# Kernel tuning notes

Hardware: AMD Instinct MI355X
Metric: run time of the kernel (lower is better)

## Reference

```python
import jax, jax.numpy as jnp
import numpy as np

B, S, D = 2, 2048, 1024
H = 16
DH = D // H  # 64

def setup_inputs() -> dict:
    key = jax.random.key(0)
    k1, k2, k3, k4 = jax.random.split(key, 4)
    scale = 0.02
    x = jax.random.normal(k1, (B, S, D), dtype=jnp.float32)
    W_query = jax.random.normal(k2, (D, D), dtype=jnp.float32) * scale
    W_key = jax.random.normal(k3, (D, D), dtype=jnp.float32) * scale
    W_value = jax.random.normal(k4, (D, D), dtype=jnp.float32) * scale
    return {"x": x, "W_query": W_query, "W_key": W_key, "W_value": W_value}

def reference(x, W_query, W_key, W_value):
    b, n, d_in = x.shape
    # project and split heads: [b, h, n, dh]
    q = (x @ W_query).reshape(b, n, H, DH).transpose(0, 2, 1, 3)
    k = (x @ W_key).reshape(b, n, H, DH).transpose(0, 2, 1, 3)
    v = (x @ W_value).reshape(b, n, H, DH).transpose(0, 2, 1, 3)
    # raw scores, then causal mask (strict upper triangle -> -inf)
    scores = jnp.einsum('bhqd,bhkd->bhqk', q, k)
    causal = jnp.tril(jnp.ones((n, n), dtype=bool))  # True = keep
    scores = jnp.where(causal, scores, -jnp.inf)
    weights = jax.nn.softmax(scores / jnp.sqrt(jnp.float32(DH)), axis=-1)
    ctx = jnp.einsum('bhqk,bhkd->bhqd', weights, v)
    return ctx.transpose(0, 2, 1, 3).reshape(b, n, H * DH)
```

## Files before the change

### kernel.cpp

```cpp
#include <hip/hip_runtime.h>
#include <hip/hip_bf16.h>

#define S_LEN   2048
#define D_MODEL 1024
#define N_HEADS 16
#define D_HEAD  64
#define HEAD_ELEMS (2048ull * 64ull)
#define MAT_ELEMS  (4096ull * 1024ull)
#define W_ELEMS    (1024ull * 1024ull)

typedef __attribute__((ext_vector_type(8))) short short8_t;
typedef __attribute__((ext_vector_type(4))) short short4_t;
typedef __attribute__((ext_vector_type(4))) float f32x4;

__device__ __forceinline__ short f2bf(float f) {
    __hip_bfloat16 h = __float2bfloat16(f);
    union { __hip_bfloat16 h; short s; } cv;
    cv.h = h;
    return cv.s;
}

#define GLD_LDS16(gptr, lptr) \
    __builtin_amdgcn_global_load_lds( \
        (const __attribute__((address_space(1))) unsigned int*)(gptr), \
        (__attribute__((address_space(3))) unsigned int*)(lptr), 16, 0, 0)

__global__ __launch_bounds__(256) void convert_x_kernel(
    const float* __restrict__ x, short* __restrict__ xb)
{
    const int i = (blockIdx.x * 256 + threadIdx.x) * 8;
    const float4 v0 = *(const float4*)(x + i);
    const float4 v1 = *(const float4*)(x + i + 4);
    short8_t u;
    u[0] = f2bf(v0.x); u[1] = f2bf(v0.y); u[2] = f2bf(v0.z); u[3] = f2bf(v0.w);
    u[4] = f2bf(v1.x); u[5] = f2bf(v1.y); u[6] = f2bf(v1.z); u[7] = f2bf(v1.w);
    *(short8_t*)(xb + i) = u;
}

__global__ __launch_bounds__(256) void transpose_w_kernel(
    const float* __restrict__ Wq, const float* __restrict__ Wk,
    const float* __restrict__ Wv, short* __restrict__ wt)
{
    const int k0 = blockIdx.x * 64;
    const int n0 = blockIdx.y * 64;
    const int which = blockIdx.z;
    const float* W = (which == 0) ? Wq : (which == 1) ? Wk : Wv;
    short* out = wt + (size_t)which * W_ELEMS;

    __shared__ float Ts[64][68];
    const int t = threadIdx.x;
    {
        const int c4 = (t & 15) * 4;
#pragma unroll
        for (int i = 0; i < 4; ++i) {
            const int r = (t >> 4) + i * 16;
            const float4 v = *(const float4*)(W + (size_t)(k0 + r) * D_MODEL + n0 + c4);
            Ts[c4 + 0][r] = v.x; Ts[c4 + 1][r] = v.y;
            Ts[c4 + 2][r] = v.z; Ts[c4 + 3][r] = v.w;
        }
    }
    __syncthreads();
    const int nl = t >> 2;
#pragma unroll
    for (int s = 0; s < 2; ++s) {
        const int koff = (t & 3) * 8 + s * 32;
        short8_t u;
#pragma unroll
        for (int j = 0; j < 8; ++j) u[j] = f2bf(Ts[nl][koff + j]);
        *(short8_t*)(out + (size_t)(n0 + nl) * D_MODEL + k0 + koff) = u;
    }
}

__global__ __launch_bounds__(256, 3) void qkv_mfma_gemm_kernel(
    const short* __restrict__ xb,
    const short* __restrict__ wt,
    short* __restrict__ qkv)
{
    const int mBlock = blockIdx.x * 128;
    const int nBlock = blockIdx.y * 128;
    const int which  = blockIdx.z;
    const short* Bt = wt + (size_t)which * W_ELEMS;
    short* outBase  = qkv + (size_t)which * MAT_ELEMS;

    __shared__ short As[128 * 32];
    __shared__ short Bs[128 * 32];

    const int t    = threadIdx.x;
    const int w    = t >> 6;
    const int lane = t & 63;
    const int n16  = lane & 15;
    const int quad = lane >> 4;
    const int mq   = (w & 1) * 64;
    const int nq   = (w >> 1) * 64;

    f32x4 acc[4][4];
#pragma unroll
    for (int i = 0; i < 4; ++i)
#pragma unroll
        for (int j = 0; j < 4; ++j) acc[i][j] = (f32x4){0.f, 0.f, 0.f, 0.f};

    const int off0 = w * 2048 + lane * 16;
    const int off1 = off0 + 1024;
    const int r0s = off0 >> 6, k0s = (off0 & 63) >> 1;
    const int r1s = off1 >> 6, k1s = (off1 & 63) >> 1;
    const short* gA0 = xb + (size_t)(mBlock + r0s) * D_MODEL + k0s;
    const short* gA1 = xb + (size_t)(mBlock + r1s) * D_MODEL + k1s;
    const short* gB0 = Bt + (size_t)(nBlock + r0s) * D_MODEL + k0s;
    const short* gB1 = Bt + (size_t)(nBlock + r1s) * D_MODEL + k1s;
    short* lA0 = As + w * 1024;
    short* lA1 = As + w * 1024 + 512;
    short* lB0 = Bs + w * 1024;
    short* lB1 = Bs + w * 1024 + 512;

    for (int k0 = 0; k0 < D_MODEL; k0 += 32) {
        __syncthreads();
        GLD_LDS16(gA0 + k0, lA0);
        GLD_LDS16(gA1 + k0, lA1);
        GLD_LDS16(gB0 + k0, lB0);
        GLD_LDS16(gB1 + k0, lB1);
        __syncthreads();

        short8_t af[4], bf[4];
#pragma unroll
        for (int mt = 0; mt < 4; ++mt)
            af[mt] = *(const short8_t*)&As[(mq + mt * 16 + n16) * 32 + quad * 8];
#pragma unroll
        for (int nt = 0; nt < 4; ++nt)
            bf[nt] = *(const short8_t*)&Bs[(nq + nt * 16 + n16) * 32 + quad * 8];
#pragma unroll
        for (int mt = 0; mt < 4; ++mt)
#pragma unroll
            for (int nt = 0; nt < 4; ++nt)
                acc[mt][nt] = __builtin_amdgcn_mfma_f32_16x16x32_bf16(
                    af[mt], bf[nt], acc[mt][nt], 0, 0, 0);
    }

    const float oscale = (which == 0) ? 0.125f : 1.0f;
    if (which < 2) {
#pragma unroll
        for (int mt = 0; mt < 4; ++mt) {
#pragma unroll
            for (int nt = 0; nt < 4; ++nt) {
                const int n = nBlock + nq + nt * 16 + n16;
                const int h = n >> 6, dh = n & 63;
#pragma unroll
                for (int reg = 0; reg < 4; ++reg) {
                    const int m = mBlock + mq + mt * 16 + quad * 4 + reg;
                    const int bb = m >> 11, ss = m & 2047;
                    outBase[((size_t)(bb * N_HEADS + h) * S_LEN + ss) * D_HEAD + dh] =
                        f2bf(acc[mt][nt][reg] * oscale);
                }
            }
        }
    } else {
#pragma unroll
        for (int mt = 0; mt < 4; ++mt) {
            const int m0 = mBlock + mq + mt * 16 + quad * 4;
            const int bb = m0 >> 11, ss0 = m0 & 2047;
#pragma unroll
            for (int nt = 0; nt < 4; ++nt) {
                const int n = nBlock + nq + nt * 16 + n16;
                const int h = n >> 6, dh = n & 63;
                short4_t u;
                u[0] = f2bf(acc[mt][nt][0]); u[1] = f2bf(acc[mt][nt][1]);
                u[2] = f2bf(acc[mt][nt][2]); u[3] = f2bf(acc[mt][nt][3]);
                *(short4_t*)(outBase +
                    ((size_t)((bb * N_HEADS + h) * D_HEAD + dh)) * S_LEN + ss0) = u;
            }
        }
    }
}

__global__ __launch_bounds__(256, 2) void attn_mfma_kernel(
    const short* __restrict__ qkv,
    float* __restrict__ out)
{
    const int bh   = blockIdx.x;
    const int pr   = blockIdx.y;
    const int t    = threadIdx.x;
    const int w    = t >> 6;
    const int lane = t & 63;
    const int n    = lane & 15;
    const int quad = lane >> 4;

    const short* Q  = qkv + (size_t)bh * HEAD_ELEMS;
    const short* K  = qkv + MAT_ELEMS + (size_t)bh * HEAD_ELEMS;
    const short* Vt = qkv + 2 * MAT_ELEMS + (size_t)bh * HEAD_ELEMS;

    __shared__ __align__(16) short Ks[64 * 64];
    __shared__ __align__(16) short Vs[64 * 64];
    __shared__ __align__(16) short Ps[4][16][72];

    const int srow0 = w * 16 + (lane >> 3);
    const int srow1 = srow0 + 8;
    const int sd0 = ((lane & 7) ^ (srow0 & 7)) * 8;
    const int sd1 = ((lane & 7) ^ (srow1 & 7)) * 8;
    const short* gK0 = K + srow0 * 64 + sd0;
    const short* gK1 = K + srow1 * 64 + sd1;
    const short* gV0 = Vt + (size_t)srow0 * S_LEN + sd0;
    const short* gV1 = Vt + (size_t)srow1 * S_LEN + sd1;
    short* lK0 = Ks + (w * 16) * 64;
    short* lK1 = Ks + (w * 16 + 8) * 64;
    short* lV0 = Vs + (w * 16) * 64;
    short* lV1 = Vs + (w * 16 + 8) * 64;

    const int pcK = ((quad ^ (n & 7))) * 8;

    const int bb = bh >> 4;
    const int hh = bh & 15;

    for (int pass = 0; pass < 2; ++pass) {
        const int qb = pass ? (31 - pr) : pr;
        const int r0 = qb * 64 + w * 16;
        const int qrow = r0 + n;

        const short8_t bq0 = *(const short8_t*)(Q + (size_t)qrow * D_HEAD + quad * 8);
        const short8_t bq1 = *(const short8_t*)(Q + (size_t)qrow * D_HEAD + quad * 8 + 32);

        float m = -__builtin_inff();
        float l = 0.f;
        f32x4 o[4];
#pragma unroll
        for (int f = 0; f < 4; ++f) o[f] = (f32x4){0.f, 0.f, 0.f, 0.f};

        for (int tile = 0; tile <= qb; ++tile) {
            const int j0 = tile * 64;
            __syncthreads();
            GLD_LDS16(gK0 + j0 * 64, lK0);
            GLD_LDS16(gK1 + j0 * 64, lK1);
            GLD_LDS16(gV0 + j0, lV0);
            GLD_LDS16(gV1 + j0, lV1);
            __syncthreads();

            f32x4 st[4];
#pragma unroll
            for (int kg = 0; kg < 4; ++kg) {
                const int rbase = (kg * 16 + n) * 64;
                const short8_t a0 = *(const short8_t*)&Ks[rbase + pcK];
                const short8_t a1 = *(const short8_t*)&Ks[rbase + (pcK ^ 32)];
                f32x4 acc = (f32x4){0.f, 0.f, 0.f, 0.f};
                acc = __builtin_amdgcn_mfma_f32_16x16x32_bf16(a0, bq0, acc, 0, 0, 0);
                acc = __builtin_amdgcn_mfma_f32_16x16x32_bf16(a1, bq1, acc, 0, 0, 0);
                st[kg] = acc;
            }

            float p[16];
            float mx = -__builtin_inff();
            if (tile == qb) {
#pragma unroll
                for (int kg = 0; kg < 4; ++kg)
#pragma unroll
                    for (int r = 0; r < 4; ++r) {
                        const int key = j0 + kg * 16 + quad * 4 + r;
                        float s = st[kg][r];
                        s = (key <= qrow) ? s : -__builtin_inff();
                        p[kg * 4 + r] = s;
                        mx = fmaxf(mx, s);
                    }
            } else {
#pragma unroll
                for (int i = 0; i < 16; ++i) {
                    const float s = st[i >> 2][i & 3];
                    p[i] = s;
                    mx = fmaxf(mx, s);
                }
            }
            mx = fmaxf(mx, __shfl_xor(mx, 16));
            mx = fmaxf(mx, __shfl_xor(mx, 32));
            const float mnew  = fmaxf(m, mx);
            const float alpha = __expf(m - mnew);
            float ls = 0.f;
#pragma unroll
            for (int i = 0; i < 16; ++i) {
                p[i] = __expf(p[i] - mnew);
                ls += p[i];
            }
            ls += __shfl_xor(ls, 16);
            ls += __shfl_xor(ls, 32);
            l = l * alpha + ls;
            m = mnew;
#pragma unroll
            for (int f = 0; f < 4; ++f) {
                o[f][0] *= alpha; o[f][1] *= alpha; o[f][2] *= alpha; o[f][3] *= alpha;
            }

#pragma unroll
            for (int kg = 0; kg < 4; ++kg) {
                const unsigned int b0 = __builtin_bit_cast(unsigned int, p[kg * 4 + 0]);
                const unsigned int b1 = __builtin_bit_cast(unsigned int, p[kg * 4 + 1]);
                const unsigned int b2 = __builtin_bit_cast(unsigned int, p[kg * 4 + 2]);
                const unsigned int b3 = __builtin_bit_cast(unsigned int, p[kg * 4 + 3]);
                uint2 pk;
                pk.x = (b0 >> 16) | (b1 & 0xffff0000u);
                pk.y = (b2 >> 16) | (b3 & 0xffff0000u);
                *(uint2*)&Ps[w][n][kg * 16 + quad * 4] = pk;
            }
            const short8_t pb0 = *(const short8_t*)&Ps[w][n][quad * 8];
            const short8_t pb1 = *(const short8_t*)&Ps[w][n][quad * 8 + 32];

#pragma unroll
            for (int f = 0; f < 4; ++f) {
                const int rbase = (f * 16 + n) * 64;
                const short8_t va0 = *(const short8_t*)&Vs[rbase + pcK];
                const short8_t va1 = *(const short8_t*)&Vs[rbase + (pcK ^ 32)];
                o[f] = __builtin_amdgcn_mfma_f32_16x16x32_bf16(va0, pb0, o[f], 0, 0, 0);
                o[f] = __builtin_amdgcn_mfma_f32_16x16x32_bf16(va1, pb1, o[f], 0, 0, 0);
            }
        }

        __syncthreads();
        float* Os = (float*)((w < 2) ? Ks : Vs) + (w & 1) * 1024;
        const float inv_l = 1.0f / l;
#pragma unroll
        for (int f = 0; f < 4; ++f) {
            const int c  = f * 4 + quad;
            const int pc = c ^ n;
            f32x4 q4;
            q4[0] = o[f][0] * inv_l; q4[1] = o[f][1] * inv_l;
            q4[2] = o[f][2] * inv_l; q4[3] = o[f][3] * inv_l;
            *(f32x4*)&Os[n * 64 + pc * 4] = q4;
        }
#pragma unroll
        for (int rr = 0; rr < 4; ++rr) {
            const int row = rr * 4 + quad;
            const int pc  = n ^ row;
            const f32x4 val = *(const f32x4*)&Os[row * 64 + pc * 4];
            *(f32x4*)(out + ((size_t)(bb * S_LEN + r0 + row)) * D_MODEL
                          + hh * D_HEAD + n * 4) = val;
        }
    }
}

extern "C" void kernel_launch(void* const* d_in, const int* in_sizes, int n_in,
                              void* d_out, int out_size, void* d_ws, size_t ws_size,
                              hipStream_t stream) {
    const float* x  = (const float*)d_in[0];
    const float* Wq = (const float*)d_in[1];
    const float* Wk = (const float*)d_in[2];
    const float* Wv = (const float*)d_in[3];
    float* out = (float*)d_out;

    short* xb  = (short*)d_ws;
    short* wt  = xb + MAT_ELEMS;
    short* qkv = wt + 3 * W_ELEMS;

    convert_x_kernel<<<dim3(MAT_ELEMS / (256 * 8)), 256, 0, stream>>>(x, xb);
    transpose_w_kernel<<<dim3(16, 16, 3), 256, 0, stream>>>(Wq, Wk, Wv, wt);

    qkv_mfma_gemm_kernel<<<dim3(32, 8, 3), 256, 0, stream>>>(xb, wt, qkv);

    attn_mfma_kernel<<<dim3(2 * N_HEADS, 16), 256, 0, stream>>>(qkv, out);
}
```

Baseline: 155.0 us.

## Stage QK epilogue through LDS, fold log2e into Q, lazy softmax rescale, one tile per block

The Q/K projection epilogue now writes each wave's 64x64 tile into padded LDS and then stores contiguous 16-byte rows to global memory, replacing scattered 2-byte stores. The 1/sqrt(d) scale is multiplied by log2(e) and baked into Q so softmax can use exp2 directly. A lazy-rescale branch skips the max update and the accumulator rescale while the new tile max stays within 8 of the running max. The attention grid changes from 16 blocks each running two paired query tiles to 32 blocks each running one tile, with launch bounds raised to 4 blocks per CU and s_setprio around the MFMA sections. Together these aim to cut store traffic, exponent cost and rescale work and to raise occupancy, at the cost of 36 KB more LDS in the GEMM and losing the paired-tile load balancing.

```diff
diff --git a/kernel.cpp b/kernel.cpp
--- a/kernel.cpp
+++ b/kernel.cpp
@@ -84,6 +84,7 @@
 
     __shared__ short As[128 * 32];
     __shared__ short Bs[128 * 32];
+    __shared__ __align__(16) short Es[4][64 * 72];
 
     const int t    = threadIdx.x;
     const int w    = t >> 6;
@@ -135,22 +136,32 @@
                     af[mt], bf[nt], acc[mt][nt], 0, 0, 0);
     }
 
-    const float oscale = (which == 0) ? 0.125f : 1.0f;
+    const float oscale = (which == 0) ? 0.125f * 1.44269504089f : 1.0f;
     if (which < 2) {
-#pragma unroll
-        for (int mt = 0; mt < 4; ++mt) {
+        short* E = &Es[w][0];
+#pragma unroll
+        for (int mt = 0; mt < 4; ++mt)
 #pragma unroll
             for (int nt = 0; nt < 4; ++nt) {
-                const int n = nBlock + nq + nt * 16 + n16;
-                const int h = n >> 6, dh = n & 63;
+                const int dhl = nt * 16 + n16;
 #pragma unroll
                 for (int reg = 0; reg < 4; ++reg) {
-                    const int m = mBlock + mq + mt * 16 + quad * 4 + reg;
-                    const int bb = m >> 11, ss = m & 2047;
-                    outBase[((size_t)(bb * N_HEADS + h) * S_LEN + ss) * D_HEAD + dh] =
-                        f2bf(acc[mt][nt][reg] * oscale);
+                    const int ml = mt * 16 + quad * 4 + reg;
+                    E[ml * 72 + dhl] = f2bf(acc[mt][nt][reg] * oscale);
                 }
             }
+        const int h  = (nBlock + nq) >> 6;
+        const int m0 = mBlock + mq;
+        const int bb = m0 >> 11, ss0 = m0 & 2047;
+        const int rsub = lane >> 3;
+        const int ch   = lane & 7;
+        short* orow = outBase + ((size_t)(bb * N_HEADS + h) * S_LEN + ss0) * D_HEAD
+                      + ch * 8;
+#pragma unroll
+        for (int it = 0; it < 8; ++it) {
+            const int row = it * 8 + rsub;
+            const short8_t v = *(const short8_t*)&E[row * 72 + ch * 8];
+            *(short8_t*)(orow + (size_t)row * D_HEAD) = v;
         }
     } else {
 #pragma unroll
@@ -171,12 +182,12 @@
     }
 }
 
-__global__ __launch_bounds__(256, 2) void attn_mfma_kernel(
+__global__ __launch_bounds__(256, 4) void attn_mfma_kernel(
     const short* __restrict__ qkv,
     float* __restrict__ out)
 {
     const int bh   = blockIdx.x;
-    const int pr   = blockIdx.y;
+    const int qb   = 31 - blockIdx.y;
     const int t    = threadIdx.x;
     const int w    = t >> 6;
     const int lane = t & 63;
@@ -209,70 +220,81 @@
     const int bb = bh >> 4;
     const int hh = bh & 15;
 
-    for (int pass = 0; pass < 2; ++pass) {
-        const int qb = pass ? (31 - pr) : pr;
-        const int r0 = qb * 64 + w * 16;
-        const int qrow = r0 + n;
-
-        const short8_t bq0 = *(const short8_t*)(Q + (size_t)qrow * D_HEAD + quad * 8);
-        const short8_t bq1 = *(const short8_t*)(Q + (size_t)qrow * D_HEAD + quad * 8 + 32);
-
-        float m = -__builtin_inff();
-        float l = 0.f;
-        f32x4 o[4];
-#pragma unroll
-        for (int f = 0; f < 4; ++f) o[f] = (f32x4){0.f, 0.f, 0.f, 0.f};
-
-        for (int tile = 0; tile <= qb; ++tile) {
-            const int j0 = tile * 64;
-            __syncthreads();
-            GLD_LDS16(gK0 + j0 * 64, lK0);
-            GLD_LDS16(gK1 + j0 * 64, lK1);
-            GLD_LDS16(gV0 + j0, lV0);
-            GLD_LDS16(gV1 + j0, lV1);
-            __syncthreads();
-
-            f32x4 st[4];
-#pragma unroll
-            for (int kg = 0; kg < 4; ++kg) {
-                const int rbase = (kg * 16 + n) * 64;
-                const short8_t a0 = *(const short8_t*)&Ks[rbase + pcK];
-                const short8_t a1 = *(const short8_t*)&Ks[rbase + (pcK ^ 32)];
-                f32x4 acc = (f32x4){0.f, 0.f, 0.f, 0.f};
-                acc = __builtin_amdgcn_mfma_f32_16x16x32_bf16(a0, bq0, acc, 0, 0, 0);
-                acc = __builtin_amdgcn_mfma_f32_16x16x32_bf16(a1, bq1, acc, 0, 0, 0);
-                st[kg] = acc;
-            }
-
-            float p[16];
-            float mx = -__builtin_inff();
-            if (tile == qb) {
-#pragma unroll
-                for (int kg = 0; kg < 4; ++kg)
-#pragma unroll
-                    for (int r = 0; r < 4; ++r) {
-                        const int key = j0 + kg * 16 + quad * 4 + r;
-                        float s = st[kg][r];
-                        s = (key <= qrow) ? s : -__builtin_inff();
-                        p[kg * 4 + r] = s;
-                        mx = fmaxf(mx, s);
-                    }
-            } else {
-#pragma unroll
-                for (int i = 0; i < 16; ++i) {
-                    const float s = st[i >> 2][i & 3];
-                    p[i] = s;
+    const int r0   = qb * 64 + w * 16;
+    const int qrow = r0 + n;
+
+    const short8_t bq0 = *(const short8_t*)(Q + (size_t)qrow * D_HEAD + quad * 8);
+    const short8_t bq1 = *(const short8_t*)(Q + (size_t)qrow * D_HEAD + quad * 8 + 32);
+
+    float m = -__builtin_inff();
+    float l = 0.f;
+    f32x4 o[4];
+#pragma unroll
+    for (int f = 0; f < 4; ++f) o[f] = (f32x4){0.f, 0.f, 0.f, 0.f};
+
+    for (int tile = 0; tile <= qb; ++tile) {
+        const int j0 = tile * 64;
+        __syncthreads();
+        GLD_LDS16(gK0 + j0 * 64, lK0);
+        GLD_LDS16(gK1 + j0 * 64, lK1);
+        GLD_LDS16(gV0 + j0, lV0);
+        GLD_LDS16(gV1 + j0, lV1);
+        __syncthreads();
+
+        f32x4 st[4];
+        __builtin_amdgcn_s_setprio(1);
+#pragma unroll
+        for (int kg = 0; kg < 4; ++kg) {
+            const int rbase = (kg * 16 + n) * 64;
+            const short8_t a0 = *(const short8_t*)&Ks[rbase + pcK];
+            const short8_t a1 = *(const short8_t*)&Ks[rbase + (pcK ^ 32)];
+            f32x4 acc = (f32x4){0.f, 0.f, 0.f, 0.f};
+            acc = __builtin_amdgcn_mfma_f32_16x16x32_bf16(a0, bq0, acc, 0, 0, 0);
+            acc = __builtin_amdgcn_mfma_f32_16x16x32_bf16(a1, bq1, acc, 0, 0, 0);
+            st[kg] = acc;
+        }
+        __builtin_amdgcn_s_setprio(0);
+
+        float p[16];
+        float mx = -__builtin_inff();
+        if (tile == qb) {
+#pragma unroll
+            for (int kg = 0; kg < 4; ++kg)
+#pragma unroll
+                for (int r = 0; r < 4; ++r) {
+                    const int key = j0 + kg * 16 + quad * 4 + r;
+                    float s = st[kg][r];
+                    s = (key <= qrow) ? s : -__builtin_inff();
+                    p[kg * 4 + r] = s;
                     mx = fmaxf(mx, s);
                 }
-            }
-            mx = fmaxf(mx, __shfl_xor(mx, 16));
-            mx = fmaxf(mx, __shfl_xor(mx, 32));
+        } else {
+#pragma unroll
+            for (int i = 0; i < 16; ++i) {
+                const float s = st[i >> 2][i & 3];
+                p[i] = s;
+                mx = fmaxf(mx, s);
+            }
+        }
+        mx = fmaxf(mx, __shfl_xor(mx, 16));
+        mx = fmaxf(mx, __shfl_xor(mx, 32));
+
+        float ls = 0.f;
+        if (__all(mx <= m + 8.0f)) {
+#pragma unroll
+            for (int i = 0; i < 16; ++i) {
+                p[i] = __builtin_amdgcn_exp2f(p[i] - m);
+                ls += p[i];
+            }
+            ls += __shfl_xor(ls, 16);
+            ls += __shfl_xor(ls, 32);
+            l += ls;
+        } else {
             const float mnew  = fmaxf(m, mx);
-            const float alpha = __expf(m - mnew);
-            float ls = 0.f;
+            const float alpha = __builtin_amdgcn_exp2f(m - mnew);
 #pragma unroll
             for (int i = 0; i < 16; ++i) {
-                p[i] = __expf(p[i] - mnew);
+                p[i] = __builtin_amdgcn_exp2f(p[i] - mnew);
                 ls += p[i];
             }
             ls += __shfl_xor(ls, 16);
@@ -281,53 +303,56 @@
             m = mnew;
 #pragma unroll
             for (int f = 0; f < 4; ++f) {
-                o[f][0] *= alpha; o[f][1] *= alpha; o[f][2] *= alpha; o[f][3] *= alpha;
-            }
-
-#pragma unroll
-            for (int kg = 0; kg < 4; ++kg) {
-                const unsigned int b0 = __builtin_bit_cast(unsigned int, p[kg * 4 + 0]);
-                const unsigned int b1 = __builtin_bit_cast(unsigned int, p[kg * 4 + 1]);
-                const unsigned int b2 = __builtin_bit_cast(unsigned int, p[kg * 4 + 2]);
-                const unsigned int b3 = __builtin_bit_cast(unsigned int, p[kg * 4 + 3]);
-                uint2 pk;
-                pk.x = (b0 >> 16) | (b1 & 0xffff0000u);
-                pk.y = (b2 >> 16) | (b3 & 0xffff0000u);
-                *(uint2*)&Ps[w][n][kg * 16 + quad * 4] = pk;
-            }
-            const short8_t pb0 = *(const short8_t*)&Ps[w][n][quad * 8];
-            const short8_t pb1 = *(const short8_t*)&Ps[w][n][quad * 8 + 32];
-
-#pragma unroll
-            for (int f = 0; f < 4; ++f) {
-                const int rbase = (f * 16 + n) * 64;
-                const short8_t va0 = *(const short8_t*)&Vs[rbase + pcK];
-                const short8_t va1 = *(const short8_t*)&Vs[rbase + (pcK ^ 32)];
-                o[f] = __builtin_amdgcn_mfma_f32_16x16x32_bf16(va0, pb0, o[f], 0, 0, 0);
-                o[f] = __builtin_amdgcn_mfma_f32_16x16x32_bf16(va1, pb1, o[f], 0, 0, 0);
-            }
-        }
-
-        __syncthreads();
-        float* Os = (float*)((w < 2) ? Ks : Vs) + (w & 1) * 1024;
-        const float inv_l = 1.0f / l;
+                o[f][0] *= alpha; o[f][1] *= alpha;
+                o[f][2] *= alpha; o[f][3] *= alpha;
+            }
+        }
+
+#pragma unroll
+        for (int kg = 0; kg < 4; ++kg) {
+            const unsigned int b0 = __builtin_bit_cast(unsigned int, p[kg * 4 + 0]);
+            const unsigned int b1 = __builtin_bit_cast(unsigned int, p[kg * 4 + 1]);
+            const unsigned int b2 = __builtin_bit_cast(unsigned int, p[kg * 4 + 2]);
+            const unsigned int b3 = __builtin_bit_cast(unsigned int, p[kg * 4 + 3]);
+            uint2 pk;
+            pk.x = (b0 >> 16) | (b1 & 0xffff0000u);
+            pk.y = (b2 >> 16) | (b3 & 0xffff0000u);
+            *(uint2*)&Ps[w][n][kg * 16 + quad * 4] = pk;
+        }
+        const short8_t pb0 = *(const short8_t*)&Ps[w][n][quad * 8];
+        const short8_t pb1 = *(const short8_t*)&Ps[w][n][quad * 8 + 32];
+
+        __builtin_amdgcn_s_setprio(1);
 #pragma unroll
         for (int f = 0; f < 4; ++f) {
-            const int c  = f * 4 + quad;
-            const int pc = c ^ n;
-            f32x4 q4;
-            q4[0] = o[f][0] * inv_l; q4[1] = o[f][1] * inv_l;
-            q4[2] = o[f][2] * inv_l; q4[3] = o[f][3] * inv_l;
-            *(f32x4*)&Os[n * 64 + pc * 4] = q4;
-        }
-#pragma unroll
-        for (int rr = 0; rr < 4; ++rr) {
-            const int row = rr * 4 + quad;
-            const int pc  = n ^ row;
-            const f32x4 val = *(const f32x4*)&Os[row * 64 + pc * 4];
-            *(f32x4*)(out + ((size_t)(bb * S_LEN + r0 + row)) * D_MODEL
-                          + hh * D_HEAD + n * 4) = val;
-        }
+            const int rbase = (f * 16 + n) * 64;
+            const short8_t va0 = *(const short8_t*)&Vs[rbase + pcK];
+            const short8_t va1 = *(const short8_t*)&Vs[rbase + (pcK ^ 32)];
+            o[f] = __builtin_amdgcn_mfma_f32_16x16x32_bf16(va0, pb0, o[f], 0, 0, 0);
+            o[f] = __builtin_amdgcn_mfma_f32_16x16x32_bf16(va1, pb1, o[f], 0, 0, 0);
+        }
+        __builtin_amdgcn_s_setprio(0);
+    }
+
+    __syncthreads();
+    float* Os = (float*)((w < 2) ? (void*)Ks : (void*)Vs) + (w & 1) * 1024;
+    const float inv_l = 1.0f / l;
+#pragma unroll
+    for (int f = 0; f < 4; ++f) {
+        const int c  = f * 4 + quad;
+        const int pc = c ^ n;
+        f32x4 q4;
+        q4[0] = o[f][0] * inv_l; q4[1] = o[f][1] * inv_l;
+        q4[2] = o[f][2] * inv_l; q4[3] = o[f][3] * inv_l;
+        *(f32x4*)&Os[n * 64 + pc * 4] = q4;
+    }
+#pragma unroll
+    for (int rr = 0; rr < 4; ++rr) {
+        const int row = rr * 4 + quad;
+        const int pc  = n ^ row;
+        const f32x4 val = *(const f32x4*)&Os[row * 64 + pc * 4];
+        *(f32x4*)(out + ((size_t)(bb * S_LEN + r0 + row)) * D_MODEL
+                      + hh * D_HEAD + n * 4) = val;
     }
 }
 
@@ -349,5 +374,5 @@
 
     qkv_mfma_gemm_kernel<<<dim3(32, 8, 3), 256, 0, stream>>>(xb, wt, qkv);
 
-    attn_mfma_kernel<<<dim3(2 * N_HEADS, 16), 256, 0, stream>>>(qkv, out);
-}
+    attn_mfma_kernel<<<dim3(32, 32), 256, 0, stream>>>(qkv, out);
+}
```

Result: no change. 155.1 us (+0.1%).
